# Performance work log

Hardware: AMD Instinct MI355X
Metric: run time of the kernel (lower is better)

Reference implementation:

```python
import jax, jax.numpy as jnp
import numpy as np

B, S, H, NH = 2, 2048, 2048, 16
HD = H // NH  # 128
SCALE = HD ** -0.5


def rotate_half(x):
    x1, x2 = x[..., : x.shape[-1] // 2], x[..., x.shape[-1] // 2 :]
    return jnp.concatenate((-x2, x1), axis=-1)


def setup_inputs() -> dict:
    key = jax.random.key(0)
    ks = jax.random.split(key, 7)
    inv_freq = 1.0 / (10000.0 ** (np.arange(0, HD, 2, dtype=np.float32) / HD))
    t = np.arange(S, dtype=np.float32)
    freqs = np.outer(t, inv_freq)  # [S, HD/2]
    emb = np.concatenate([freqs, freqs], axis=-1)  # [S, HD]
    cos = jnp.asarray(np.cos(emb))[None, None]  # [1,1,S,HD]
    sin = jnp.asarray(np.sin(emb))[None, None]
    std = H ** -0.5
    return {
        "hidden_states": jax.random.normal(ks[0], (B, S, H), jnp.float32),
        "cos": cos,
        "sin": sin,
        "Wq": jax.random.normal(ks[1], (H, H), jnp.float32) * std,
        "Wk": jax.random.normal(ks[2], (H, H), jnp.float32) * std,
        "Wv": jax.random.normal(ks[3], (H, H), jnp.float32) * std,
        "Wo": jax.random.normal(ks[4], (H, H), jnp.float32) * std,
    }


def reference(hidden_states, cos, sin, Wq, Wk, Wv, Wo):
    b, s, _ = hidden_states.shape
    # projections (torch F.linear: x @ W.T), reshape to [b, nh, s, hd]
    def proj(W):
        y = jnp.einsum("bsh,oh->bso", hidden_states, W)
        return y.reshape(b, s, NH, HD).transpose(0, 2, 1, 3)

    q, k, v = proj(Wq), proj(Wk), proj(Wv)
    # rotary embedding
    q = q * cos + rotate_half(q) * sin
    k = k * cos + rotate_half(k) * sin
    # attention: scores [b, nh, s, s]
    scores = jnp.einsum("bhqd,bhkd->bhqk", q, k) * SCALE
    causal_mask = jnp.triu(jnp.full((s, s), -jnp.inf, dtype=scores.dtype), k=1)
    scores = scores + causal_mask
    attn = jax.nn.softmax(scores, axis=-1)
    out = jnp.einsum("bhqk,bhkd->bhqd", attn, v)
    out = out.transpose(0, 2, 1, 3).reshape(b, s, NH * HD)
    return jnp.einsum("bso,ho->bsh", out, Wo)
```

## Files before the change

kernel.cpp:

```cpp
#include <hip/hip_runtime.h>

typedef unsigned short u16;
typedef unsigned int   u32;
typedef __attribute__((ext_vector_type(8))) __bf16 bf16x8;
typedef __attribute__((ext_vector_type(8))) unsigned short u16x8;
typedef __attribute__((ext_vector_type(4))) float f32x4;

#define DEVINL static __device__ __forceinline__
#define MFMA16(a,b,c) __builtin_amdgcn_mfma_f32_16x16x32_bf16((a),(b),(c),0,0,0)

#define GLOAD16(g, l) __builtin_amdgcn_global_load_lds( \
    (const __attribute__((address_space(1))) void*)(g), \
    (__attribute__((address_space(3))) void*)(l), 16, 0, 0)

constexpr float ATT_SCALE = 0.08838834764831845f;

DEVINL u16 f2bf(float f) {
  union { float f; u32 u; } v; v.f = f;
  u32 r = v.u + 0x7fffu + ((v.u >> 16) & 1u);
  return (u16)(r >> 16);
}

struct CvtArgs {
  const float* src[5];
  u16*         dst[5];
  int          nblk[5];
};

__global__ __launch_bounds__(256) void cvt_bf16(CvtArgs a) {
  const int z = blockIdx.y;
  if (blockIdx.x >= a.nblk[z]) return;
  const size_t i = ((size_t)blockIdx.x * 256 + threadIdx.x) * 8;
  const float* s = a.src[z] + i;
  float4 x0 = *(const float4*)(s);
  float4 x1 = *(const float4*)(s + 4);
  u16x8 r;
  r[0]=f2bf(x0.x); r[1]=f2bf(x0.y); r[2]=f2bf(x0.z); r[3]=f2bf(x0.w);
  r[4]=f2bf(x1.x); r[5]=f2bf(x1.y); r[6]=f2bf(x1.z); r[7]=f2bf(x1.w);
  *(u16x8*)(a.dst[z] + i) = r;
}

template<int EPI>
__global__ __launch_bounds__(256)
void gemm_nt(const u16* __restrict__ A, const u16* __restrict__ W,
             void* __restrict__ outp, const float* __restrict__ cosp,
             const float* __restrict__ sinp)
{
  __shared__ __attribute__((aligned(16))) u16 Alds[128*32];
  __shared__ __attribute__((aligned(16))) u16 Blds[128*32];
  __shared__ __attribute__((aligned(16))) u16 vtbuf[(EPI==1) ? 128*136 : 16];

  const int t    = threadIdx.x;
  const int bm   = blockIdx.x, bn = blockIdx.y;
  const int lane = t & 63, w = t >> 6;
  const int c    = lane & 15, qq = lane >> 4;

  f32x4 acc[2][8] = {};

  for (int kt = 0; kt < 64; ++kt) {
    __syncthreads();
    #pragma unroll
    for (int i = 0; i < 2; ++i) {
      const int chunk = i*256 + t;
      const int row   = chunk >> 2;
      const int seg   = chunk & 3;
      const u16* ga = A + (size_t)(bm*128 + row)*2048 + kt*32 + seg*8;
      GLOAD16(ga, &Alds[(size_t)chunk*8]);
      const u16* gb = W + (size_t)(bn*128 + row)*2048 + kt*32 + seg*8;
      GLOAD16(gb, &Blds[(size_t)chunk*8]);
    }
    __syncthreads();

    bf16x8 a0 = *(const bf16x8*)&Alds[(w*32 +  0 + c)*32 + qq*8];
    bf16x8 a1 = *(const bf16x8*)&Alds[(w*32 + 16 + c)*32 + qq*8];
    #pragma unroll
    for (int nj = 0; nj < 8; ++nj) {
      bf16x8 bv = *(const bf16x8*)&Blds[(nj*16 + c)*32 + qq*8];
      acc[0][nj] = MFMA16(a0, bv, acc[0][nj]);
      acc[1][nj] = MFMA16(a1, bv, acc[1][nj]);
    }
  }

  if (EPI == 2) {
    float* out = (float*)outp;
    #pragma unroll
    for (int mi = 0; mi < 2; ++mi)
      #pragma unroll
      for (int nj = 0; nj < 8; ++nj)
        #pragma unroll
        for (int r = 0; r < 4; ++r) {
          int row = bm*128 + w*32 + mi*16 + qq*4 + r;
          int col = bn*128 + nj*16 + c;
          out[(size_t)row*2048 + col] = acc[mi][nj][r];
        }
  } else if (EPI == 0) {
    u16* qk = (u16*)outp;
    #pragma unroll
    for (int mi = 0; mi < 2; ++mi)
      #pragma unroll
      for (int r = 0; r < 4; ++r) {
        int m  = bm*128 + w*32 + mi*16 + qq*4 + r;
        int bb = m >> 11, s = m & 2047;
        const float* cs = cosp + s*128;
        const float* sn = sinp + s*128;
        u16* orow = qk + ((size_t)(bb*16 + bn)*2048 + s)*128;
        #pragma unroll
        for (int nj = 0; nj < 4; ++nj) {
          int d1 = nj*16 + c, d2 = d1 + 64;
          float v1 = acc[mi][nj][r], v2 = acc[mi][nj+4][r];
          orow[d1] = f2bf(v1*cs[d1] - v2*sn[d1]);
          orow[d2] = f2bf(v2*cs[d2] + v1*sn[d2]);
        }
      }
  } else {
    #pragma unroll
    for (int mi = 0; mi < 2; ++mi)
      #pragma unroll
      for (int nj = 0; nj < 8; ++nj)
        #pragma unroll
        for (int r = 0; r < 4; ++r)
          vtbuf[(nj*16 + c)*136 + w*32 + mi*16 + qq*4 + r] = f2bf(acc[mi][nj][r]);
    __syncthreads();
    int bb = bm >> 4;
    int s0 = (bm & 15) * 128;
    const int drow = t >> 1;
    const int half = (t & 1) * 64;
    u16* og = (u16*)outp + ((size_t)(bb*16 + bn)*128 + drow)*2048 + s0 + half;
    #pragma unroll
    for (int j = 0; j < 8; ++j)
      *(u16x8*)&og[j*8] = *(const u16x8*)&vtbuf[drow*136 + half + j*8];
  }
}

__global__ __launch_bounds__(256, 2)
void attn_fwd(const u16* __restrict__ qw, const u16* __restrict__ kw,
              const u16* __restrict__ vw, u16* __restrict__ ow)
{
  __shared__ __attribute__((aligned(16))) u16 Klds[2][64*128];
  __shared__ __attribute__((aligned(16))) u16 Vlds[2][128*64];
  __shared__ __attribute__((aligned(16))) u16 Plds[4][16*72];

  const int t = threadIdx.x, lane = t & 63, w = t >> 6;
  const int c = lane & 15, qq = lane >> 4;
  const int ip = blockIdx.x, h = blockIdx.y, b = blockIdx.z;
  const int qlo = ip, qhi = 31 - ip;

  const size_t bh = (size_t)b*16 + h;
  const u16* Qg = qw + bh*(2048*128);
  const u16* Kg = kw + bh*(2048*128);
  const u16* Vg = vw + bh*(128*2048);
  u16* pw = &Plds[w][0];

  bf16x8 qf_hi[4], qf_lo[4];
  {
    const u16* qh = Qg + (size_t)(qhi*64 + w*16 + c)*128;
    const u16* ql = Qg + (size_t)(qlo*64 + w*16 + c)*128;
    #pragma unroll
    for (int ds = 0; ds < 4; ++ds) {
      qf_hi[ds] = *(const bf16x8*)(qh + ds*32 + qq*8);
      qf_lo[ds] = *(const bf16x8*)(ql + ds*32 + qq*8);
    }
  }

  float m_hi[4] = {-1e30f,-1e30f,-1e30f,-1e30f};
  float l_hi[4] = {0.f,0.f,0.f,0.f};
  f32x4 o_hi[8] = {};
  float m_lo[4] = {-1e30f,-1e30f,-1e30f,-1e30f};
  float l_lo[4] = {0.f,0.f,0.f,0.f};
  f32x4 o_lo[8] = {};

#define STAGE(BUF, KT) do {                                                   \
    const u16* kbase = Kg + (size_t)(KT)*8192;                                \
    _Pragma("unroll")                                                         \
    for (int it = 0; it < 4; ++it) {                                          \
      const u32 p  = it*256 + t;                                              \
      const u32 gl = p ^ ((p >> 4) & 7u);                                     \
      GLOAD16(kbase + gl*8, &Klds[BUF][p*8]);                                 \
    }                                                                         \
    _Pragma("unroll")                                                         \
    for (int it = 0; it < 4; ++it) {                                          \
      const u32 p  = it*256 + t;                                              \
      const u32 gl = p ^ ((p >> 3) & 7u);                                     \
      GLOAD16(Vg + (size_t)(gl >> 3)*2048 + (KT)*64 + (gl & 7u)*8,            \
              &Vlds[BUF][p*8]);                                               \
    }                                                                         \
  } while (0)

#define PROCESS(QF, OACC, MR, LR, QBASE, DIAG, BUF) do {                      \
    f32x4 sc[4] = {};                                                         \
    __builtin_amdgcn_s_setprio(1);                                            \
    _Pragma("unroll")                                                         \
    for (int ds = 0; ds < 4; ++ds) {                                          \
      _Pragma("unroll")                                                       \
      for (int nj = 0; nj < 4; ++nj) {                                        \
        const u32 row = nj*16 + c;                                            \
        const u32 p = (row*128 + ds*32 + qq*8) ^ ((row & 7u) << 3);           \
        bf16x8 kb = *(const bf16x8*)&Klds[BUF][p];                            \
        sc[nj] = MFMA16(QF[ds], kb, sc[nj]);                                  \
      }                                                                       \
    }                                                                         \
    __builtin_amdgcn_s_setprio(0);                                            \
    const int qg0 = (QBASE) + w*16 + qq*4;                                    \
    float escale[4];                                                          \
    _Pragma("unroll")                                                         \
    for (int r = 0; r < 4; ++r) {                                             \
      float mx = -1e30f;                                                      \
      _Pragma("unroll")                                                       \
      for (int nj = 0; nj < 4; ++nj) {                                        \
        float s = sc[nj][r] * ATT_SCALE;                                      \
        if ((DIAG) && (kt*64 + nj*16 + c) > (qg0 + r)) s = -1e30f;            \
        sc[nj][r] = s;                                                        \
        mx = fmaxf(mx, s);                                                    \
      }                                                                       \
      mx = fmaxf(mx, __shfl_xor(mx, 1));                                      \
      mx = fmaxf(mx, __shfl_xor(mx, 2));                                      \
      mx = fmaxf(mx, __shfl_xor(mx, 4));                                      \
      mx = fmaxf(mx, __shfl_xor(mx, 8));                                      \
      float mnew = fmaxf(MR[r], mx);                                          \
      escale[r] = __expf(MR[r] - mnew);                                       \
      MR[r] = mnew;                                                           \
      float sum = 0.f;                                                        \
      _Pragma("unroll")                                                       \
      for (int nj = 0; nj < 4; ++nj) {                                        \
        float pv = __expf(sc[nj][r] - mnew);                                  \
        sum += pv;                                                            \
        pw[(qq*4 + r)*72 + nj*16 + c] = f2bf(pv);                             \
      }                                                                       \
      sum += __shfl_xor(sum, 1);                                              \
      sum += __shfl_xor(sum, 2);                                              \
      sum += __shfl_xor(sum, 4);                                              \
      sum += __shfl_xor(sum, 8);                                              \
      LR[r] = LR[r]*escale[r] + sum;                                          \
    }                                                                         \
    _Pragma("unroll")                                                         \
    for (int nj8 = 0; nj8 < 8; ++nj8)                                         \
      _Pragma("unroll")                                                       \
      for (int r = 0; r < 4; ++r)                                             \
        OACC[nj8][r] *= escale[r];                                            \
    __builtin_amdgcn_s_setprio(1);                                            \
    _Pragma("unroll")                                                         \
    for (int ks = 0; ks < 2; ++ks) {                                          \
      bf16x8 pa = *(const bf16x8*)&pw[c*72 + ks*32 + qq*8];                   \
      _Pragma("unroll")                                                       \
      for (int nj8 = 0; nj8 < 8; ++nj8) {                                     \
        const u32 row = nj8*16 + c;                                           \
        const u32 p = (row*64 + ks*32 + qq*8) ^ ((row & 7u) << 3);            \
        bf16x8 vb = *(const bf16x8*)&Vlds[BUF][p];                            \
        OACC[nj8] = MFMA16(pa, vb, OACC[nj8]);                                \
      }                                                                       \
    }                                                                         \
    __builtin_amdgcn_s_setprio(0);                                            \
  } while (0)

  STAGE(0, 0);
  for (int kt = 0; kt <= qhi; ++kt) {
    const int cur = kt & 1;
    __syncthreads();
    if (kt < qhi) STAGE(cur ^ 1, kt + 1);
    PROCESS(qf_hi, o_hi, m_hi, l_hi, qhi*64, (kt == qhi), cur);
    if (kt <= qlo)
      PROCESS(qf_lo, o_lo, m_lo, l_lo, qlo*64, (kt == qlo), cur);
  }

#undef STAGE
#undef PROCESS

  {
    float inv[4];
    #pragma unroll
    for (int r = 0; r < 4; ++r) inv[r] = 1.0f / l_hi[r];
    u16* og = ow + ((size_t)b*2048 + qhi*64 + w*16)*2048 + h*128;
    #pragma unroll
    for (int nj8 = 0; nj8 < 8; ++nj8)
      #pragma unroll
      for (int r = 0; r < 4; ++r)
        og[(size_t)(qq*4 + r)*2048 + nj8*16 + c] = f2bf(o_hi[nj8][r]*inv[r]);
  }
  {
    float inv[4];
    #pragma unroll
    for (int r = 0; r < 4; ++r) inv[r] = 1.0f / l_lo[r];
    u16* og = ow + ((size_t)b*2048 + qlo*64 + w*16)*2048 + h*128;
    #pragma unroll
    for (int nj8 = 0; nj8 < 8; ++nj8)
      #pragma unroll
      for (int r = 0; r < 4; ++r)
        og[(size_t)(qq*4 + r)*2048 + nj8*16 + c] = f2bf(o_lo[nj8][r]*inv[r]);
  }
}

extern "C" void kernel_launch(void* const* d_in, const int* in_sizes, int n_in,
                              void* d_out, int out_size, void* d_ws, size_t ws_size,
                              hipStream_t stream)
{
  const float* hs   = (const float*)d_in[0];
  const float* cosp = (const float*)d_in[1];
  const float* sinp = (const float*)d_in[2];
  const float* Wq   = (const float*)d_in[3];
  const float* Wk   = (const float*)d_in[4];
  const float* Wv   = (const float*)d_in[5];
  const float* Wo   = (const float*)d_in[6];

  u16* q_ws  = (u16*)d_ws;
  u16* k_ws  = q_ws  + 8388608;
  u16* vt_ws = k_ws  + 8388608;
  u16* ao_ws = vt_ws + 8388608;
  u16* hs_b  = ao_ws + 8388608;
  u16* wq_b  = hs_b  + 8388608;
  u16* wk_b  = wq_b  + 4194304;
  u16* wv_b  = wk_b  + 4194304;
  u16* wo_b  = wv_b  + 4194304;

  CvtArgs ca;
  ca.src[0]=hs; ca.src[1]=Wq; ca.src[2]=Wk; ca.src[3]=Wv; ca.src[4]=Wo;
  ca.dst[0]=hs_b; ca.dst[1]=wq_b; ca.dst[2]=wk_b; ca.dst[3]=wv_b; ca.dst[4]=wo_b;
  ca.nblk[0]=4096; ca.nblk[1]=2048; ca.nblk[2]=2048; ca.nblk[3]=2048; ca.nblk[4]=2048;

  dim3 blk(256);
  cvt_bf16<<<dim3(4096, 5), blk, 0, stream>>>(ca);

  dim3 g(32, 16);
  gemm_nt<0><<<g, blk, 0, stream>>>(hs_b, wq_b, q_ws,  cosp, sinp);
  gemm_nt<0><<<g, blk, 0, stream>>>(hs_b, wk_b, k_ws,  cosp, sinp);
  gemm_nt<1><<<g, blk, 0, stream>>>(hs_b, wv_b, vt_ws, nullptr, nullptr);
  attn_fwd<<<dim3(16, 16, 2), blk, 0, stream>>>(q_ws, k_ws, vt_ws, ao_ws);
  gemm_nt<2><<<g, blk, 0, stream>>>(ao_ws, wo_b, d_out, nullptr, nullptr);
}
```

Before: 435.0 us.

## Replace projection GEMMs with 256x128 triple-buffered 8-wave GEMM and fuse QKV launches

The old 128x128 single-buffered GEMM is replaced by a 512-thread kernel that computes 256x128 tiles with a K-tile of 64. It uses a three-slot LDS ring with XOR-swizzled layout, and its phases interleave global-to-LDS staging with MFMA work under explicit waitcnt and barriers. The Q, K and V projections are merged into one launch, with the weight matrix picked by grid y, while keeping the RoPE and V-transpose epilogues. The intent is to hide memory latency, increase data reuse per tile and cut launch count. The cost is one block per CU and more complex manual synchronisation.

```diff
diff --git a/kernel.cpp b/kernel.cpp
--- a/kernel.cpp
+++ b/kernel.cpp
@@ -40,95 +40,145 @@
   *(u16x8*)(a.dst[z] + i) = r;
 }
 
-template<int EPI>
-__global__ __launch_bounds__(256)
-void gemm_nt(const u16* __restrict__ A, const u16* __restrict__ W,
-             void* __restrict__ outp, const float* __restrict__ cosp,
-             const float* __restrict__ sinp)
+#define SLOT_U16 24576
+#define A_HALF_U16 8192
+#define B_OFF_U16 16384
+#define B_HALF_U16 4096
+
+#define STAGE_AH(s, half, ktile) do {                                          \
+    _Pragma("unroll")                                                          \
+    for (int it_ = 0; it_ < 2; ++it_) {                                        \
+      const u32 p_  = it_*512 + t;                                             \
+      const u32 gl_ = p_ ^ ((p_ >> 3) & 7u);                                   \
+      GLOAD16(A + (size_t)(bm*256 + (half)*128 + (gl_ >> 3))*2048              \
+                 + (ktile)*64 + (gl_ & 7u)*8,                                  \
+              &lds[(s)*SLOT_U16 + (half)*A_HALF_U16 + p_*8]);                  \
+    } } while (0)
+
+#define STAGE_BH(s, half, ktile) do {                                          \
+    const u32 p_  = (u32)t;                                                    \
+    const u32 gl_ = p_ ^ ((p_ >> 3) & 7u);                                     \
+    GLOAD16(Wg + (size_t)(bnl*128 + (half)*64 + (gl_ >> 3))*2048               \
+               + (ktile)*64 + (gl_ & 7u)*8,                                    \
+            &lds[(s)*SLOT_U16 + B_OFF_U16 + (half)*B_HALF_U16 + p_*8]);        \
+  } while (0)
+
+#define LDA(s, mfg, ks) (*(const bf16x8*)&lds[(s)*SLOT_U16 + wm*A_HALF_U16 +   \
+    ((((mfg)*16 + c)*64 + (ks)*32 + qq*8) ^ ((u32)(c & 7) << 3))])
+#define LDB(s, nf, ks)  (*(const bf16x8*)&lds[(s)*SLOT_U16 + B_OFF_U16 +       \
+    (nf)*B_HALF_U16 + (((wn*16 + c)*64 + (ks)*32 + qq*8) ^ ((u32)(c & 7) << 3))])
+
+#define PHASE(s, mq, ks, LOADB, VMW, ...) do {                                 \
+    if (LOADB) { bfr0 = LDB(s, 0, ks); bfr1 = LDB(s, 1, ks); }                 \
+    bf16x8 a0_ = LDA(s, (mq)*4+0, ks);                                         \
+    bf16x8 a1_ = LDA(s, (mq)*4+1, ks);                                         \
+    bf16x8 a2_ = LDA(s, (mq)*4+2, ks);                                         \
+    bf16x8 a3_ = LDA(s, (mq)*4+3, ks);                                         \
+    __VA_ARGS__;                                                               \
+    if (VMW) { asm volatile("s_waitcnt vmcnt(6)" ::: "memory"); }              \
+    __builtin_amdgcn_s_barrier();                                              \
+    asm volatile("s_waitcnt lgkmcnt(0)" ::: "memory");                         \
+    __builtin_amdgcn_sched_barrier(0);                                         \
+    __builtin_amdgcn_s_setprio(1);                                             \
+    acc[(mq)*4+0][0] = MFMA16(a0_, bfr0, acc[(mq)*4+0][0]);                    \
+    acc[(mq)*4+1][0] = MFMA16(a1_, bfr0, acc[(mq)*4+1][0]);                    \
+    acc[(mq)*4+2][0] = MFMA16(a2_, bfr0, acc[(mq)*4+2][0]);                    \
+    acc[(mq)*4+3][0] = MFMA16(a3_, bfr0, acc[(mq)*4+3][0]);                    \
+    acc[(mq)*4+0][1] = MFMA16(a0_, bfr1, acc[(mq)*4+0][1]);                    \
+    acc[(mq)*4+1][1] = MFMA16(a1_, bfr1, acc[(mq)*4+1][1]);                    \
+    acc[(mq)*4+2][1] = MFMA16(a2_, bfr1, acc[(mq)*4+2][1]);                    \
+    acc[(mq)*4+3][1] = MFMA16(a3_, bfr1, acc[(mq)*4+3][1]);                    \
+    __builtin_amdgcn_s_setprio(0);                                             \
+    __builtin_amdgcn_s_barrier();                                              \
+  } while (0)
+
+template<int FUSED>
+__global__ __launch_bounds__(512, 1)
+void gemm8(const u16* __restrict__ A, const u16* __restrict__ W0,
+           const u16* __restrict__ W1, const u16* __restrict__ W2,
+           u16* __restrict__ outq, u16* __restrict__ outk,
+           u16* __restrict__ outv, float* __restrict__ outf,
+           const float* __restrict__ cosp, const float* __restrict__ sinp)
 {
-  __shared__ __attribute__((aligned(16))) u16 Alds[128*32];
-  __shared__ __attribute__((aligned(16))) u16 Blds[128*32];
-  __shared__ __attribute__((aligned(16))) u16 vtbuf[(EPI==1) ? 128*136 : 16];
-
-  const int t    = threadIdx.x;
-  const int bm   = blockIdx.x, bn = blockIdx.y;
+  __shared__ __attribute__((aligned(16))) u16 lds[3*SLOT_U16];
+
+  const int t = threadIdx.x;
   const int lane = t & 63, w = t >> 6;
-  const int c    = lane & 15, qq = lane >> 4;
-
-  f32x4 acc[2][8] = {};
-
-  for (int kt = 0; kt < 64; ++kt) {
-    __syncthreads();
-    #pragma unroll
-    for (int i = 0; i < 2; ++i) {
-      const int chunk = i*256 + t;
-      const int row   = chunk >> 2;
-      const int seg   = chunk & 3;
-      const u16* ga = A + (size_t)(bm*128 + row)*2048 + kt*32 + seg*8;
-      GLOAD16(ga, &Alds[(size_t)chunk*8]);
-      const u16* gb = W + (size_t)(bn*128 + row)*2048 + kt*32 + seg*8;
-      GLOAD16(gb, &Blds[(size_t)chunk*8]);
-    }
-    __syncthreads();
-
-    bf16x8 a0 = *(const bf16x8*)&Alds[(w*32 +  0 + c)*32 + qq*8];
-    bf16x8 a1 = *(const bf16x8*)&Alds[(w*32 + 16 + c)*32 + qq*8];
-    #pragma unroll
-    for (int nj = 0; nj < 8; ++nj) {
-      bf16x8 bv = *(const bf16x8*)&Blds[(nj*16 + c)*32 + qq*8];
-      acc[0][nj] = MFMA16(a0, bv, acc[0][nj]);
-      acc[1][nj] = MFMA16(a1, bv, acc[1][nj]);
-    }
-  }
-
-  if (EPI == 2) {
-    float* out = (float*)outp;
-    #pragma unroll
-    for (int mi = 0; mi < 2; ++mi)
-      #pragma unroll
-      for (int nj = 0; nj < 8; ++nj)
+  const int wm = w >> 2, wn = w & 3;
+  const int c = lane & 15, qq = lane >> 4;
+  const int bm = blockIdx.x, bn = blockIdx.y;
+  const int z   = FUSED ? (bn >> 4) : 3;
+  const int bnl = FUSED ? (bn & 15) : bn;
+  const u16* Wg = FUSED ? (z == 0 ? W0 : (z == 1 ? W1 : W2)) : W0;
+
+  f32x4 acc[8][2] = {};
+
+  STAGE_AH(0, 0, 0); STAGE_AH(0, 1, 0); STAGE_BH(0, 0, 0); STAGE_BH(0, 1, 0);
+  STAGE_AH(1, 0, 1); STAGE_AH(1, 1, 1); STAGE_BH(1, 0, 1); STAGE_BH(1, 1, 1);
+  asm volatile("s_waitcnt vmcnt(6)" ::: "memory");
+  __builtin_amdgcn_s_barrier();
+
+  bf16x8 bfr0, bfr1;
+  int slot = 0;
+  #pragma unroll 1
+  for (int i = 0; i < 32; ++i) {
+    const int s2 = (slot >= 1) ? slot - 1 : 2;
+    const int tn = (i < 30) ? i + 2 : 31;
+    PHASE(slot, 0, 0, 1, 0, STAGE_AH(s2, 0, tn));
+    PHASE(slot, 1, 0, 0, 0, STAGE_AH(s2, 1, tn));
+    PHASE(slot, 0, 1, 1, 0, STAGE_BH(s2, 0, tn); STAGE_BH(s2, 1, tn));
+    PHASE(slot, 1, 1, 0, 1, );
+    slot = (slot == 2) ? 0 : slot + 1;
+  }
+
+  __syncthreads();
+
+  if (!FUSED) {
+    #pragma unroll
+    for (int mfg = 0; mfg < 8; ++mfg)
+      #pragma unroll
+      for (int nf = 0; nf < 2; ++nf)
         #pragma unroll
         for (int r = 0; r < 4; ++r) {
-          int row = bm*128 + w*32 + mi*16 + qq*4 + r;
-          int col = bn*128 + nj*16 + c;
-          out[(size_t)row*2048 + col] = acc[mi][nj][r];
+          int row = bm*256 + wm*128 + mfg*16 + qq*4 + r;
+          int col = bnl*128 + nf*64 + wn*16 + c;
+          outf[(size_t)row*2048 + col] = acc[mfg][nf][r];
         }
-  } else if (EPI == 0) {
-    u16* qk = (u16*)outp;
-    #pragma unroll
-    for (int mi = 0; mi < 2; ++mi)
+    return;
+  }
+
+  if (z <= 1) {
+    u16* qk = (z == 0) ? outq : outk;
+    const int d1 = wn*16 + c, d2 = d1 + 64;
+    #pragma unroll
+    for (int mfg = 0; mfg < 8; ++mfg)
       #pragma unroll
       for (int r = 0; r < 4; ++r) {
-        int m  = bm*128 + w*32 + mi*16 + qq*4 + r;
+        int m  = bm*256 + wm*128 + mfg*16 + qq*4 + r;
         int bb = m >> 11, s = m & 2047;
         const float* cs = cosp + s*128;
         const float* sn = sinp + s*128;
-        u16* orow = qk + ((size_t)(bb*16 + bn)*2048 + s)*128;
-        #pragma unroll
-        for (int nj = 0; nj < 4; ++nj) {
-          int d1 = nj*16 + c, d2 = d1 + 64;
-          float v1 = acc[mi][nj][r], v2 = acc[mi][nj+4][r];
-          orow[d1] = f2bf(v1*cs[d1] - v2*sn[d1]);
-          orow[d2] = f2bf(v2*cs[d2] + v1*sn[d2]);
-        }
+        u16* orow = qk + ((size_t)(bb*16 + bnl)*2048 + s)*128;
+        float v1 = acc[mfg][0][r], v2 = acc[mfg][1][r];
+        orow[d1] = f2bf(v1*cs[d1] - v2*sn[d1]);
+        orow[d2] = f2bf(v2*cs[d2] + v1*sn[d2]);
       }
   } else {
     #pragma unroll
-    for (int mi = 0; mi < 2; ++mi)
-      #pragma unroll
-      for (int nj = 0; nj < 8; ++nj)
+    for (int mfg = 0; mfg < 8; ++mfg)
+      #pragma unroll
+      for (int nf = 0; nf < 2; ++nf)
         #pragma unroll
         for (int r = 0; r < 4; ++r)
-          vtbuf[(nj*16 + c)*136 + w*32 + mi*16 + qq*4 + r] = f2bf(acc[mi][nj][r]);
+          lds[(nf*64 + wn*16 + c)*264 + wm*128 + mfg*16 + qq*4 + r] =
+              f2bf(acc[mfg][nf][r]);
     __syncthreads();
-    int bb = bm >> 4;
-    int s0 = (bm & 15) * 128;
-    const int drow = t >> 1;
-    const int half = (t & 1) * 64;
-    u16* og = (u16*)outp + ((size_t)(bb*16 + bn)*128 + drow)*2048 + s0 + half;
+    const int d = t >> 2, seg = t & 3;
+    const int bb = bm >> 3, s0 = (bm & 7) * 256;
+    u16* og = outv + ((size_t)(bb*16 + bnl)*128 + d)*2048 + s0 + seg*64;
     #pragma unroll
     for (int j = 0; j < 8; ++j)
-      *(u16x8*)&og[j*8] = *(const u16x8*)&vtbuf[drow*136 + half + j*8];
+      *(u16x8*)&og[j*8] = *(const u16x8*)&lds[d*264 + seg*64 + j*8];
   }
 }
 
@@ -169,7 +219,7 @@
   float l_lo[4] = {0.f,0.f,0.f,0.f};
   f32x4 o_lo[8] = {};
 
-#define STAGE(BUF, KT) do {                                                   \
+#define ASTAGE(BUF, KT) do {                                                  \
     const u16* kbase = Kg + (size_t)(KT)*8192;                                \
     _Pragma("unroll")                                                         \
     for (int it = 0; it < 4; ++it) {                                          \
@@ -186,7 +236,7 @@
     }                                                                         \
   } while (0)
 
-#define PROCESS(QF, OACC, MR, LR, QBASE, DIAG, BUF) do {                      \
+#define APROCESS(QF, OACC, MR, LR, QBASE, DIAG, BUF) do {                     \
     f32x4 sc[4] = {};                                                         \
     __builtin_amdgcn_s_setprio(1);                                            \
     _Pragma("unroll")                                                         \
@@ -252,18 +302,18 @@
     __builtin_amdgcn_s_setprio(0);                                            \
   } while (0)
 
-  STAGE(0, 0);
+  ASTAGE(0, 0);
   for (int kt = 0; kt <= qhi; ++kt) {
     const int cur = kt & 1;
     __syncthreads();
-    if (kt < qhi) STAGE(cur ^ 1, kt + 1);
-    PROCESS(qf_hi, o_hi, m_hi, l_hi, qhi*64, (kt == qhi), cur);
+    if (kt < qhi) ASTAGE(cur ^ 1, kt + 1);
+    APROCESS(qf_hi, o_hi, m_hi, l_hi, qhi*64, (kt == qhi), cur);
     if (kt <= qlo)
-      PROCESS(qf_lo, o_lo, m_lo, l_lo, qlo*64, (kt == qlo), cur);
-  }
-
-#undef STAGE
-#undef PROCESS
+      APROCESS(qf_lo, o_lo, m_lo, l_lo, qlo*64, (kt == qlo), cur);
+  }
+
+#undef ASTAGE
+#undef APROCESS
 
   {
     float inv[4];
@@ -316,13 +366,14 @@
   ca.dst[0]=hs_b; ca.dst[1]=wq_b; ca.dst[2]=wk_b; ca.dst[3]=wv_b; ca.dst[4]=wo_b;
   ca.nblk[0]=4096; ca.nblk[1]=2048; ca.nblk[2]=2048; ca.nblk[3]=2048; ca.nblk[4]=2048;
 
-  dim3 blk(256);
-  cvt_bf16<<<dim3(4096, 5), blk, 0, stream>>>(ca);
-
-  dim3 g(32, 16);
-  gemm_nt<0><<<g, blk, 0, stream>>>(hs_b, wq_b, q_ws,  cosp, sinp);
-  gemm_nt<0><<<g, blk, 0, stream>>>(hs_b, wk_b, k_ws,  cosp, sinp);
-  gemm_nt<1><<<g, blk, 0, stream>>>(hs_b, wv_b, vt_ws, nullptr, nullptr);
-  attn_fwd<<<dim3(16, 16, 2), blk, 0, stream>>>(q_ws, k_ws, vt_ws, ao_ws);
-  gemm_nt<2><<<g, blk, 0, stream>>>(ao_ws, wo_b, d_out, nullptr, nullptr);
-}
+  cvt_bf16<<<dim3(4096, 5), dim3(256), 0, stream>>>(ca);
+
+  gemm8<1><<<dim3(16, 48), dim3(512), 0, stream>>>(
+      hs_b, wq_b, wk_b, wv_b, q_ws, k_ws, vt_ws, nullptr, cosp, sinp);
+
+  attn_fwd<<<dim3(16, 16, 2), dim3(256), 0, stream>>>(q_ws, k_ws, vt_ws, ao_ws);
+
+  gemm8<0><<<dim3(16, 16), dim3(512), 0, stream>>>(
+      ao_ws, wo_b, nullptr, nullptr, nullptr, nullptr, nullptr,
+      (float*)d_out, nullptr, nullptr);
+}
```

Measured after the change: 399.0 us. 1.09x faster.
